# Optimization experiments

Hardware: AMD Instinct MI355X
Metric: run time of the kernel (lower is better)

## Reference

```python
import jax, jax.numpy as jnp
import numpy as np

R, S, RO, H, KD, VD = 14, 2, 7, 8, 32, 64  # resolution, stride, res_out, heads, key_dim, val_dim
EPS = 1e-5
SCALE = KD ** -0.5


def _bias_idxs():
    i = np.arange(R)
    kp = np.stack(np.meshgrid(i, i, indexing='ij')).reshape(2, -1)          # (2, 196)
    qi = np.arange(0, R, S)
    qp = np.stack(np.meshgrid(qi, qi, indexing='ij')).reshape(2, -1)        # (2, 49)
    rel = np.abs(qp[:, :, None] - kp[:, None, :])                           # (2, 49, 196)
    return jnp.asarray(rel[0] * R + rel[1], dtype=jnp.int32)                # (49, 196)

BIAS_IDXS = _bias_idxs()


def linear_norm(x, w, g, b, m, v):
    # Linear (no bias) followed by BatchNorm1d in eval mode (running stats)
    inv = g * jax.lax.rsqrt(v + EPS)
    return (x @ w.T) * inv + (b - m * inv)


def hardswish(x):
    return x * jnp.clip(x + 3.0, 0.0, 6.0) * (1.0 / 6.0)


def setup_inputs() -> dict:
    key = jax.random.key(0)
    ks = jax.random.split(key, 12)
    d = {
        'x': jax.random.normal(ks[0], (256, 196, 256), jnp.float32),
        'kv_w': jax.random.normal(ks[1], (768, 256), jnp.float32) * 0.02,
        'kv_g': jax.random.uniform(ks[2], (768,), jnp.float32, 0.5, 1.5),
        'kv_b': jax.random.normal(ks[3], (768,), jnp.float32) * 0.02,
        'kv_m': jax.random.normal(ks[4], (768,), jnp.float32) * 0.01,
        'kv_v': jax.random.uniform(ks[5], (768,), jnp.float32, 0.5, 1.5),
        'q_w': jax.random.normal(ks[6], (256, 256), jnp.float32) * 0.02,
        'q_g': jax.random.uniform(ks[7], (256,), jnp.float32, 0.5, 1.5),
        'q_b': jax.random.normal(ks[8], (256,), jnp.float32) * 0.02,
        'q_m': jax.random.normal(ks[9], (256,), jnp.float32) * 0.01,
        'q_v': jax.random.uniform(ks[10], (256,), jnp.float32, 0.5, 1.5),
        'proj_w': jax.random.normal(ks[11], (384, 512), jnp.float32) * 0.02,
        'proj_g': jnp.ones((384,), jnp.float32),
        'proj_b': jnp.zeros((384,), jnp.float32),
        'proj_m': jnp.zeros((384,), jnp.float32),
        'proj_v': jnp.ones((384,), jnp.float32),
        'attn_bias': jax.random.normal(jax.random.fold_in(key, 99), (H, R * R), jnp.float32) * 0.02,
    }
    return d


def reference(x, kv_w, kv_g, kv_b, kv_m, kv_v,
              q_w, q_g, q_b, q_m, q_v,
              proj_w, proj_g, proj_b, proj_m, proj_v, attn_bias):
    B, N, C = x.shape  # (B, 196, 256)
    kv = linear_norm(x, kv_w, kv_g, kv_b, kv_m, kv_v)          # (B, N, 768)
    kv = kv.reshape(B, N, H, KD + VD)                          # per-head split
    k = kv[..., :KD].transpose(0, 2, 3, 1)                     # (B, H, KD, N)
    v = kv[..., KD:].transpose(0, 2, 1, 3)                     # (B, H, N, VD)
    # Subsample queries on the 14x14 grid with stride 2 -> 49 tokens
    xq = x.reshape(B, R, R, C)[:, ::S, ::S].reshape(B, RO * RO, C)
    q = linear_norm(xq, q_w, q_g, q_b, q_m, q_v)               # (B, 49, 256)
    q = q.reshape(B, RO * RO, H, KD).transpose(0, 2, 1, 3)     # (B, H, 49, KD)
    bias = attn_bias[:, BIAS_IDXS]                             # (H, 49, 196)
    scores = jnp.einsum('bhqd,bhdn->bhqn', q, k) * SCALE + bias
    attn = jax.nn.softmax(scores, axis=-1)                     # (B, H, 49, 196)
    out = jnp.einsum('bhqn,bhnv->bhqv', attn, v)               # (B, H, 49, VD)
    out = out.transpose(0, 2, 1, 3).reshape(B, RO * RO, H * VD)  # (B, 49, 512)
    return linear_norm(hardswish(out), proj_w, proj_g, proj_b, proj_m, proj_v)  # (B, 49, 384)
```

## Files before the change

kernel.cpp:

```cpp
#include <hip/hip_runtime.h>

#define EPS 1e-5f
#define QK_SCALE 0.17677669529663687f

typedef __attribute__((ext_vector_type(8))) short bf16x8;
typedef __attribute__((ext_vector_type(4))) float f32x4;

__device__ inline unsigned short bf16_rne(float f) {
    unsigned int u = __float_as_uint(f);
    u = u + 0x7FFFu + ((u >> 16) & 1u);
    return (unsigned short)(u >> 16);
}
__device__ inline float bf16_f(unsigned short s) {
    return __uint_as_float(((unsigned int)s) << 16);
}
__device__ inline void split1(float v, unsigned short& hi, unsigned short& lo) {
    hi = bf16_rne(v); lo = bf16_rne(v - bf16_f(hi));
}

__device__ inline unsigned int cvtpk_bf16(float a, float b) {
    unsigned int r;
    asm("v_cvt_pk_bf16_f32 %0, %1, %2" : "=v"(r) : "v"(a), "v"(b));
    return r;
}
__device__ inline void split2pk(float a, float b, unsigned int& h, unsigned int& l) {
    h = cvtpk_bf16(a, b);
    float ra = a - __uint_as_float(h << 16);
    float rb = b - __uint_as_float(h & 0xFFFF0000u);
    l = cvtpk_bf16(ra, rb);
}
__device__ inline void split4pk(float4 v, uint2& h, uint2& l) {
    unsigned int h01, l01, h23, l23;
    split2pk(v.x, v.y, h01, l01);
    split2pk(v.z, v.w, h23, l23);
    h.x = h01; h.y = h23; l.x = l01; l.y = l23;
}

#define MFMA16(a, b, c) __builtin_amdgcn_mfma_f32_16x16x32_bf16((a), (b), (c), 0, 0, 0)

__global__ __launch_bounds__(256)
void prep_split(const float* __restrict__ kv_w, const float* __restrict__ q_w,
                const float* __restrict__ pw,
                unsigned short* __restrict__ wb_hi, unsigned short* __restrict__ wb_lo,
                unsigned short* __restrict__ pw_hi, unsigned short* __restrict__ pw_lo)
{
    int i = blockIdx.x * 256 + threadIdx.x;
    if (i < 262144) {
        int c = i & 255, j = (i >> 8) & 127, h = i >> 15;
        float v = (j < 96) ? kv_w[(h * 96 + j) * 256 + c]
                           : q_w[(h * 32 + (j - 96)) * 256 + c];
        unsigned short hi, lo; split1(v, hi, lo);
        wb_hi[i] = hi; wb_lo[i] = lo;
    } else {
        int p = i - 262144;
        if (p < 196608) {
            float v = pw[p];
            unsigned short hi, lo; split1(v, hi, lo);
            pw_hi[p] = hi; pw_lo[p] = lo;
        }
    }
}

__global__ __launch_bounds__(1024, 4)
void levit_fused_attn(const float* __restrict__ x,
                      const unsigned short* __restrict__ wb_hi,
                      const unsigned short* __restrict__ wb_lo,
                      const float* __restrict__ kv_g, const float* __restrict__ kv_b,
                      const float* __restrict__ kv_m, const float* __restrict__ kv_v,
                      const float* __restrict__ q_g, const float* __restrict__ q_b,
                      const float* __restrict__ q_m, const float* __restrict__ q_v,
                      const float* __restrict__ attn_bias,
                      unsigned short* __restrict__ ao_hi,
                      unsigned short* __restrict__ ao_lo)
{
    __shared__ __align__(16) unsigned short s_big[80192];
    __shared__ float bias_s[196];
    __shared__ float nrm_iv[128];
    __shared__ float nrm_be[128];

    unsigned short* s_phi = s_big;
    unsigned short* s_plo = s_big + 14848;
    unsigned short* s_khi = s_big + 29696;
    unsigned short* s_klo = s_big + 38016;
    unsigned short* s_qhi = s_big + 46336;
    unsigned short* s_qlo = s_big + 48416;
    unsigned short* s_vhi = s_big + 50496;
    unsigned short* s_vlo = s_big + 65344;
    unsigned short* st_xhi = s_big;
    unsigned short* st_xlo = s_big + 14976;
    unsigned short* st_whi = s_big + 29952;
    unsigned short* st_wlo = s_big + 39168;

    const int t = threadIdx.x;
    const int b = blockIdx.x;
    const int hh = blockIdx.y;

    const int l = t & 63;
    const int w = t >> 6;
    const int rg = w & 3;
    const int cg = w >> 2;
    const int lrow = l & 15;
    const int kg = (l >> 4) * 8;
    const int g4 = (l >> 4) * 4;

    const int x0row = t >> 3,  x0c8 = (t & 7) * 8;
    const int u1 = t + 1024;
    const int x1row = u1 >> 3, x1c8 = (u1 & 7) * 8;
    const bool xv1 = (t < 640);
    const int wj = t >> 3, wc8 = (t & 7) * 8;
    const unsigned short* wsrc_hi = wb_hi + (hh * 128 + wj) * 256 + wc8;
    const unsigned short* wsrc_lo = wb_lo + (hh * 128 + wj) * 256 + wc8;
    const float* xbase = x + b * 196 * 256;
    const float4 f4z = {0.f, 0.f, 0.f, 0.f};

    float4 x0a, x0b, x1a, x1b; bf16x8 wrh, wrl;

    x0a = (x0row < 196) ? *(const float4*)&xbase[x0row * 256 + x0c8]     : f4z;
    x0b = (x0row < 196) ? *(const float4*)&xbase[x0row * 256 + x0c8 + 4] : f4z;
    x1a = f4z; x1b = f4z;
    if (xv1 && x1row < 196) {
        x1a = *(const float4*)&xbase[x1row * 256 + x1c8];
        x1b = *(const float4*)&xbase[x1row * 256 + x1c8 + 4];
    }
    wrh = *(const bf16x8*)&wsrc_hi[0];
    wrl = *(const bf16x8*)&wsrc_lo[0];

    if (t < 196) bias_s[t] = attn_bias[hh * 196 + t];
    if (t >= 256 && t < 384) {
        int jj = t - 256;
        float gg, bb, mm, vv;
        if (jj < 96) { int col = hh * 96 + jj;        gg = kv_g[col]; bb = kv_b[col]; mm = kv_m[col]; vv = kv_v[col]; }
        else         { int col = hh * 32 + (jj - 96); gg = q_g[col];  bb = q_b[col];  mm = q_m[col];  vv = q_v[col]; }
        float iv = gg * rsqrtf(vv + EPS);
        nrm_iv[jj] = iv; nrm_be[jj] = bb - mm * iv;
    }
    for (int i = t; i < 64 * 36; i += 1024) {
        int r = i / 36, c = 196 + i % 36;
        s_vhi[r * 232 + c] = 0; s_vlo[r * 232 + c] = 0;
    }

    f32x4 acc[4][2];
    #pragma unroll
    for (int i = 0; i < 4; ++i) { acc[i][0] = (f32x4){0,0,0,0}; acc[i][1] = (f32x4){0,0,0,0}; }

    {
        uint2 ha, la, hb, lb;
        split4pk(x0a, ha, la); split4pk(x0b, hb, lb);
        *(uint4*)&st_xhi[x0row * 72 + x0c8] = (uint4){ha.x, ha.y, hb.x, hb.y};
        *(uint4*)&st_xlo[x0row * 72 + x0c8] = (uint4){la.x, la.y, lb.x, lb.y};
        if (xv1) {
            split4pk(x1a, ha, la); split4pk(x1b, hb, lb);
            *(uint4*)&st_xhi[x1row * 72 + x1c8] = (uint4){ha.x, ha.y, hb.x, hb.y};
            *(uint4*)&st_xlo[x1row * 72 + x1c8] = (uint4){la.x, la.y, lb.x, lb.y};
        }
    }
    *(bf16x8*)&st_whi[wj * 72 + wc8] = wrh;
    *(bf16x8*)&st_wlo[wj * 72 + wc8] = wrl;
    __syncthreads();

    for (int s = 0; s < 4; ++s) {
        if (s < 3) {
            const int kcn = 64 * (s + 1);
            x0a = (x0row < 196) ? *(const float4*)&xbase[x0row * 256 + kcn + x0c8]     : f4z;
            x0b = (x0row < 196) ? *(const float4*)&xbase[x0row * 256 + kcn + x0c8 + 4] : f4z;
            x1a = f4z; x1b = f4z;
            if (xv1 && x1row < 196) {
                x1a = *(const float4*)&xbase[x1row * 256 + kcn + x1c8];
                x1b = *(const float4*)&xbase[x1row * 256 + kcn + x1c8 + 4];
            }
            wrh = *(const bf16x8*)&wsrc_hi[kcn];
            wrl = *(const bf16x8*)&wsrc_lo[kcn];
        }

        #pragma unroll
        for (int sub = 0; sub < 2; ++sub) {
            const int ko = 32 * sub + kg;
            bf16x8 wfh[2], wfl[2];
            #pragma unroll
            for (int ctl = 0; ctl < 2; ++ctl) {
                const int jr = 16 * (2 * cg + ctl) + lrow;
                wfh[ctl] = *(const bf16x8*)&st_whi[jr * 72 + ko];
                wfl[ctl] = *(const bf16x8*)&st_wlo[jr * 72 + ko];
            }
            #pragma unroll
            for (int i = 0; i < 4; ++i) {
                const int rt = rg + 4 * i;
                if (rt < 13) {
                    const int arow = 16 * rt + lrow;
                    bf16x8 xh = *(const bf16x8*)&st_xhi[arow * 72 + ko];
                    bf16x8 xl = *(const bf16x8*)&st_xlo[arow * 72 + ko];
                    #pragma unroll
                    for (int ctl = 0; ctl < 2; ++ctl) {
                        acc[i][ctl] = MFMA16(wfh[ctl], xh, acc[i][ctl]);
                        acc[i][ctl] = MFMA16(wfh[ctl], xl, acc[i][ctl]);
                        acc[i][ctl] = MFMA16(wfl[ctl], xh, acc[i][ctl]);
                    }
                }
            }
        }

        if (s < 3) {
            uint4 h0, l0, h1, l1;
            {
                uint2 ha, la, hb, lb;
                split4pk(x0a, ha, la); split4pk(x0b, hb, lb);
                h0 = (uint4){ha.x, ha.y, hb.x, hb.y};
                l0 = (uint4){la.x, la.y, lb.x, lb.y};
                if (xv1) {
                    split4pk(x1a, ha, la); split4pk(x1b, hb, lb);
                    h1 = (uint4){ha.x, ha.y, hb.x, hb.y};
                    l1 = (uint4){la.x, la.y, lb.x, lb.y};
                }
            }
            __syncthreads();
            *(uint4*)&st_xhi[x0row * 72 + x0c8] = h0;
            *(uint4*)&st_xlo[x0row * 72 + x0c8] = l0;
            if (xv1) {
                *(uint4*)&st_xhi[x1row * 72 + x1c8] = h1;
                *(uint4*)&st_xlo[x1row * 72 + x1c8] = l1;
            }
            *(bf16x8*)&st_whi[wj * 72 + wc8] = wrh;
            *(bf16x8*)&st_wlo[wj * 72 + wc8] = wrl;
            __syncthreads();
        }
    }
    __syncthreads();

    #pragma unroll
    for (int ctl = 0; ctl < 2; ++ctl) {
        const int ct = 2 * cg + ctl;
        const int j0 = 16 * ct + g4;
        const float iv0 = nrm_iv[j0+0], be0 = nrm_be[j0+0];
        const float iv1 = nrm_iv[j0+1], be1 = nrm_be[j0+1];
        const float iv2 = nrm_iv[j0+2], be2 = nrm_be[j0+2];
        const float iv3 = nrm_iv[j0+3], be3 = nrm_be[j0+3];
        #pragma unroll
        for (int i = 0; i < 4; ++i) {
            const int rt = rg + 4 * i;
            if (rt < 13) {
                const int n = 16 * rt + lrow;
                if (n < 196) {
                    float v0 = acc[i][ctl][0] * iv0 + be0;
                    float v1 = acc[i][ctl][1] * iv1 + be1;
                    float v2 = acc[i][ctl][2] * iv2 + be2;
                    float v3 = acc[i][ctl][3] * iv3 + be3;
                    unsigned int h01, l01, h23, l23;
                    split2pk(v0, v1, h01, l01);
                    split2pk(v2, v3, h23, l23);
                    if (ct < 2) {
                        *(uint2*)&s_khi[n * 40 + j0] = (uint2){h01, h23};
                        *(uint2*)&s_klo[n * 40 + j0] = (uint2){l01, l23};
                    } else if (ct < 6) {
                        const int vd0 = j0 - 32;
                        s_vhi[(vd0+0) * 232 + n] = (unsigned short)h01;
                        s_vhi[(vd0+1) * 232 + n] = (unsigned short)(h01 >> 16);
                        s_vhi[(vd0+2) * 232 + n] = (unsigned short)h23;
                        s_vhi[(vd0+3) * 232 + n] = (unsigned short)(h23 >> 16);
                        s_vlo[(vd0+0) * 232 + n] = (unsigned short)l01;
                        s_vlo[(vd0+1) * 232 + n] = (unsigned short)(l01 >> 16);
                        s_vlo[(vd0+2) * 232 + n] = (unsigned short)l23;
                        s_vlo[(vd0+3) * 232 + n] = (unsigned short)(l23 >> 16);
                    } else {
                        const int a = n / 28, rem = n - 28 * a;
                        if (rem < 14 && !(rem & 1)) {
                            const int qi = a * 7 + (rem >> 1);
                            *(uint2*)&s_qhi[qi * 40 + (j0 - 96)] = (uint2){h01, h23};
                            *(uint2*)&s_qlo[qi * 40 + (j0 - 96)] = (uint2){l01, l23};
                        }
                    }
                }
            }
        }
    }
    __syncthreads();

    for (int i = t; i < 64 * 24; i += 1024) {
        int r = i / 24, c = 208 + i % 24;
        s_phi[r * 232 + c] = 0; s_plo[r * 232 + c] = 0;
    }

    if (w < 4) {
        const int mt = w;
        bf16x8 qh = *(const bf16x8*)&s_qhi[(16 * mt + lrow) * 40 + kg];
        bf16x8 ql = *(const bf16x8*)&s_qlo[(16 * mt + lrow) * 40 + kg];
        f32x4 sv[13];
        #pragma unroll
        for (int nt = 0; nt < 13; ++nt) {
            bf16x8 kh = *(const bf16x8*)&s_khi[(16 * nt + lrow) * 40 + kg];
            bf16x8 kl = *(const bf16x8*)&s_klo[(16 * nt + lrow) * 40 + kg];
            f32x4 a = {0.f, 0.f, 0.f, 0.f};
            a = MFMA16(kh, qh, a);
            a = MFMA16(kh, ql, a);
            a = MFMA16(kl, qh, a);
            sv[nt] = a;
        }
        const int m = 16 * mt + lrow;
        const int mq = m < 49 ? m : 48;
        const int yq = (mq / 7) * 2, xq2 = (mq % 7) * 2;

        float lmax = -3.0e38f;
        #pragma unroll
        for (int nt = 0; nt < 13; ++nt) {
            #pragma unroll
            for (int reg = 0; reg < 4; ++reg) {
                const int n = 16 * nt + g4 + reg;
                float sc;
                if (n < 196) {
                    const int yk = n / 14, xk = n - 14 * yk;
                    int d0 = yq - yk;  d0 = d0 < 0 ? -d0 : d0;
                    int d1 = xq2 - xk; d1 = d1 < 0 ? -d1 : d1;
                    sc = sv[nt][reg] * QK_SCALE + bias_s[d0 * 14 + d1];
                } else {
                    sc = -1.0e30f;
                }
                sv[nt][reg] = sc;
                lmax = fmaxf(lmax, sc);
            }
        }
        lmax = fmaxf(lmax, __shfl_xor(lmax, 16, 64));
        lmax = fmaxf(lmax, __shfl_xor(lmax, 32, 64));
        float rsum = 0.f;
        #pragma unroll
        for (int nt = 0; nt < 13; ++nt)
            #pragma unroll
            for (int reg = 0; reg < 4; ++reg) {
                float p = __expf(sv[nt][reg] - lmax);
                sv[nt][reg] = p;
                rsum += p;
            }
        rsum += __shfl_xor(rsum, 16, 64);
        rsum += __shfl_xor(rsum, 32, 64);
        const float rinv = 1.f / rsum;
        #pragma unroll
        for (int nt = 0; nt < 13; ++nt) {
            unsigned int h01, l01, h23, l23;
            split2pk(sv[nt][0] * rinv, sv[nt][1] * rinv, h01, l01);
            split2pk(sv[nt][2] * rinv, sv[nt][3] * rinv, h23, l23);
            const int o = m * 232 + 16 * nt + g4;
            *(uint2*)&s_phi[o] = (uint2){h01, h23};
            *(uint2*)&s_plo[o] = (uint2){l01, l23};
        }
    }
    __syncthreads();

    {
        const int mtv = w & 3;
        const int ntv = w >> 2;
        f32x4 pacc = {0.f, 0.f, 0.f, 0.f};
        #pragma unroll
        for (int s = 0; s < 7; ++s) {
            bf16x8 ph = *(const bf16x8*)&s_phi[(16 * mtv + lrow) * 232 + 32 * s + kg];
            bf16x8 pl = *(const bf16x8*)&s_plo[(16 * mtv + lrow) * 232 + 32 * s + kg];
            bf16x8 vh = *(const bf16x8*)&s_vhi[(16 * ntv + lrow) * 232 + 32 * s + kg];
            bf16x8 vl = *(const bf16x8*)&s_vlo[(16 * ntv + lrow) * 232 + 32 * s + kg];
            pacc = MFMA16(vh, ph, pacc);
            pacc = MFMA16(vh, pl, pacc);
            pacc = MFMA16(vl, ph, pacc);
        }
        const int m = 16 * mtv + lrow;
        if (m < 49) {
            const int vd0 = 16 * ntv + g4;
            float hs0, hs1, hs2, hs3;
            { float v = pacc[0]; hs0 = v * fminf(fmaxf(v + 3.f, 0.f), 6.f) * (1.f/6.f); }
            { float v = pacc[1]; hs1 = v * fminf(fmaxf(v + 3.f, 0.f), 6.f) * (1.f/6.f); }
            { float v = pacc[2]; hs2 = v * fminf(fmaxf(v + 3.f, 0.f), 6.f) * (1.f/6.f); }
            { float v = pacc[3]; hs3 = v * fminf(fmaxf(v + 3.f, 0.f), 6.f) * (1.f/6.f); }
            unsigned int h01, l01, h23, l23;
            split2pk(hs0, hs1, h01, l01);
            split2pk(hs2, hs3, h23, l23);
            const int idx = ((b * 49 + m) * 8 + hh) * 64 + vd0;
            *(uint2*)&ao_hi[idx] = (uint2){h01, h23};
            *(uint2*)&ao_lo[idx] = (uint2){l01, l23};
        }
    }
}

__global__ __launch_bounds__(512, 6)
void levit_proj(const unsigned short* __restrict__ ao_hi,
                const unsigned short* __restrict__ ao_lo,
                const unsigned short* __restrict__ pw_hi,
                const unsigned short* __restrict__ pw_lo,
                const float* __restrict__ pg, const float* __restrict__ pb,
                const float* __restrict__ pm, const float* __restrict__ pv,
                float* __restrict__ out)
{
    __shared__ __align__(16) unsigned short s_a[2 * 64 * 72];
    __shared__ __align__(16) unsigned short s_w[2 * 96 * 72];

    unsigned short* s_ahi = s_a;          unsigned short* s_alo = s_a + 64 * 72;
    unsigned short* s_whi = s_w;          unsigned short* s_wlo = s_w + 96 * 72;

    const int t = threadIdx.x;
    const int b = blockIdx.x;
    const int cg = blockIdx.y;
    const int l = t & 63;
    const int w = t >> 6;
    const int lrow = l & 15;
    const int kg = (l >> 4) * 8;
    const int g4 = (l >> 4) * 4;

    const int ar = t >> 3, ac8 = (t & 7) * 8;
    const bool aval = (ar < 49);
    const long aoff = (long)(b * 49 + ar) * 512 + ac8;
    int wpl_[3], wr_[3], wc_[3];
    #pragma unroll
    for (int it = 0; it < 3; ++it) {
        int f = t + 512 * it;
        int plane = (f >= 768), rem = plane ? f - 768 : f;
        wpl_[it] = plane; wr_[it] = rem >> 3; wc_[it] = (rem & 7) * 8;
    }

    bf16x8 pa_h = {}, pa_l = {}, pwr[3];

    if (aval) {
        pa_h = *(const bf16x8*)&ao_hi[aoff];
        pa_l = *(const bf16x8*)&ao_lo[aoff];
    }
    #pragma unroll
    for (int it = 0; it < 3; ++it) {
        const unsigned short* src = wpl_[it] ? pw_lo : pw_hi;
        pwr[it] = *(const bf16x8*)&src[(cg * 96 + wr_[it]) * 512 + wc_[it]];
    }
    *(bf16x8*)&s_ahi[ar * 72 + ac8] = pa_h;
    *(bf16x8*)&s_alo[ar * 72 + ac8] = pa_l;
    #pragma unroll
    for (int it = 0; it < 3; ++it) {
        unsigned short* dst = wpl_[it] ? s_wlo : s_whi;
        *(bf16x8*)&dst[wr_[it] * 72 + wc_[it]] = pwr[it];
    }
    __syncthreads();

    const int mt = w & 3;
    const int ntb = 3 * (w >> 2);

    f32x4 acc[3] = {{0.f,0.f,0.f,0.f},{0.f,0.f,0.f,0.f},{0.f,0.f,0.f,0.f}};

    for (int s = 0; s < 8; ++s) {
        if (s < 7) {
            const int kc = 64 * (s + 1);
            pa_h = (bf16x8){}; pa_l = (bf16x8){};
            if (aval) {
                pa_h = *(const bf16x8*)&ao_hi[aoff + kc];
                pa_l = *(const bf16x8*)&ao_lo[aoff + kc];
            }
            #pragma unroll
            for (int it = 0; it < 3; ++it) {
                const unsigned short* src = wpl_[it] ? pw_lo : pw_hi;
                pwr[it] = *(const bf16x8*)&src[(cg * 96 + wr_[it]) * 512 + kc + wc_[it]];
            }
        }

        #pragma unroll
        for (int sub = 0; sub < 2; ++sub) {
            const int ko = 32 * sub + kg;
            bf16x8 ah = *(const bf16x8*)&s_ahi[(16 * mt + lrow) * 72 + ko];
            bf16x8 al = *(const bf16x8*)&s_alo[(16 * mt + lrow) * 72 + ko];
            #pragma unroll
            for (int i = 0; i < 3; ++i) {
                const int nt = ntb + i;
                bf16x8 bh = *(const bf16x8*)&s_whi[(16 * nt + lrow) * 72 + ko];
                bf16x8 bl = *(const bf16x8*)&s_wlo[(16 * nt + lrow) * 72 + ko];
                acc[i] = MFMA16(bh, ah, acc[i]);
                acc[i] = MFMA16(bl, ah, acc[i]);
                acc[i] = MFMA16(bh, al, acc[i]);
            }
        }

        if (s < 7) {
            __syncthreads();
            *(bf16x8*)&s_ahi[ar * 72 + ac8] = pa_h;
            *(bf16x8*)&s_alo[ar * 72 + ac8] = pa_l;
            #pragma unroll
            for (int it = 0; it < 3; ++it) {
                unsigned short* dst = wpl_[it] ? s_wlo : s_whi;
                *(bf16x8*)&dst[wr_[it] * 72 + wc_[it]] = pwr[it];
            }
            __syncthreads();
        }
    }

    const int r = 16 * mt + lrow;
    if (r < 49) {
        #pragma unroll
        for (int i = 0; i < 3; ++i) {
            const int nt = ntb + i;
            const int o0 = cg * 96 + 16 * nt + g4;
            const float4 g4v = *(const float4*)&pg[o0];
            const float4 v4v = *(const float4*)&pv[o0];
            const float4 b4v = *(const float4*)&pb[o0];
            const float4 m4v = *(const float4*)&pm[o0];
            float iv0 = g4v.x * rsqrtf(v4v.x + EPS);
            float iv1 = g4v.y * rsqrtf(v4v.y + EPS);
            float iv2 = g4v.z * rsqrtf(v4v.z + EPS);
            float iv3 = g4v.w * rsqrtf(v4v.w + EPS);
            float4 ov;
            ov.x = acc[i][0] * iv0 + (b4v.x - m4v.x * iv0);
            ov.y = acc[i][1] * iv1 + (b4v.y - m4v.y * iv1);
            ov.z = acc[i][2] * iv2 + (b4v.z - m4v.z * iv2);
            ov.w = acc[i][3] * iv3 + (b4v.w - m4v.w * iv3);
            *(float4*)&out[(b * 49 + r) * 384 + o0] = ov;
        }
    }
}

extern "C" void kernel_launch(void* const* d_in, const int* in_sizes, int n_in,
                              void* d_out, int out_size, void* d_ws, size_t ws_size,
                              hipStream_t stream) {
    const float* x     = (const float*)d_in[0];
    const float* kv_w  = (const float*)d_in[1];
    const float* kv_g  = (const float*)d_in[2];
    const float* kv_b  = (const float*)d_in[3];
    const float* kv_m  = (const float*)d_in[4];
    const float* kv_v  = (const float*)d_in[5];
    const float* q_wp  = (const float*)d_in[6];
    const float* q_g   = (const float*)d_in[7];
    const float* q_b   = (const float*)d_in[8];
    const float* q_m   = (const float*)d_in[9];
    const float* q_v   = (const float*)d_in[10];
    const float* pw    = (const float*)d_in[11];
    const float* pg    = (const float*)d_in[12];
    const float* pb    = (const float*)d_in[13];
    const float* pm    = (const float*)d_in[14];
    const float* pv    = (const float*)d_in[15];
    const float* ab    = (const float*)d_in[16];

    unsigned short* ao_hi = (unsigned short*)d_ws;
    unsigned short* ao_lo = ao_hi + 12544 * 512;
    unsigned short* wb_hi = ao_lo + 12544 * 512;
    unsigned short* wb_lo = wb_hi + 262144;
    unsigned short* pw_hi = wb_lo + 262144;
    unsigned short* pw_lo = pw_hi + 196608;

    prep_split<<<1792, 256, 0, stream>>>(kv_w, q_wp, pw, wb_hi, wb_lo, pw_hi, pw_lo);

    dim3 g1(256, 8);
    levit_fused_attn<<<g1, 1024, 0, stream>>>(x, wb_hi, wb_lo,
                                              kv_g, kv_b, kv_m, kv_v,
                                              q_g, q_b, q_m, q_v, ab, ao_hi, ao_lo);
    levit_proj<<<dim3(256, 4), 512, 0, stream>>>(ao_hi, ao_lo, pw_hi, pw_lo,
                                                 pg, pb, pm, pv, (float*)d_out);
}
```

Measured before the change: 281.9 us.

## Process two heads per block to reuse staged x tiles across heads

Each attention block now computes the KV/Q projection for two heads, staging 256 weight rows per K-step instead of 128, and the grid is halved along the head axis. This halves how often each fp32 x tile is read from global memory and split into bf16 hi/lo. The attention and PV stages then run the two heads one after another inside the block. Norm parameters are now read from global memory in the epilogue instead of being precomputed in shared memory. In exchange, the block keeps twice as many accumulators live, which raises register pressure, and the grid has fewer blocks.

```diff
diff --git a/kernel.cpp b/kernel.cpp
--- a/kernel.cpp
+++ b/kernel.cpp
@@ -74,9 +74,7 @@
                       unsigned short* __restrict__ ao_lo)
 {
     __shared__ __align__(16) unsigned short s_big[80192];
-    __shared__ float bias_s[196];
-    __shared__ float nrm_iv[128];
-    __shared__ float nrm_be[128];
+    __shared__ float bias_s[392];
 
     unsigned short* s_phi = s_big;
     unsigned short* s_plo = s_big + 14848;
@@ -89,11 +87,11 @@
     unsigned short* st_xhi = s_big;
     unsigned short* st_xlo = s_big + 14976;
     unsigned short* st_whi = s_big + 29952;
-    unsigned short* st_wlo = s_big + 39168;
+    unsigned short* st_wlo = s_big + 48384;
 
     const int t = threadIdx.x;
     const int b = blockIdx.x;
-    const int hh = blockIdx.y;
+    const int hp = blockIdx.y;
 
     const int l = t & 63;
     const int w = t >> 6;
@@ -107,13 +105,14 @@
     const int u1 = t + 1024;
     const int x1row = u1 >> 3, x1c8 = (u1 & 7) * 8;
     const bool xv1 = (t < 640);
-    const int wj = t >> 3, wc8 = (t & 7) * 8;
-    const unsigned short* wsrc_hi = wb_hi + (hh * 128 + wj) * 256 + wc8;
-    const unsigned short* wsrc_lo = wb_lo + (hh * 128 + wj) * 256 + wc8;
+    const int wj0 = t >> 3, wc8 = (t & 7) * 8;
+    const unsigned short* wsrc_hi = wb_hi + (hp * 256 + wj0) * 256 + wc8;
+    const unsigned short* wsrc_lo = wb_lo + (hp * 256 + wj0) * 256 + wc8;
     const float* xbase = x + b * 196 * 256;
     const float4 f4z = {0.f, 0.f, 0.f, 0.f};
 
-    float4 x0a, x0b, x1a, x1b; bf16x8 wrh, wrl;
+    float4 x0a, x0b, x1a, x1b;
+    bf16x8 wrh0, wrl0, wrh1, wrl1;
 
     x0a = (x0row < 196) ? *(const float4*)&xbase[x0row * 256 + x0c8]     : f4z;
     x0b = (x0row < 196) ? *(const float4*)&xbase[x0row * 256 + x0c8 + 4] : f4z;
@@ -122,26 +121,21 @@
         x1a = *(const float4*)&xbase[x1row * 256 + x1c8];
         x1b = *(const float4*)&xbase[x1row * 256 + x1c8 + 4];
     }
-    wrh = *(const bf16x8*)&wsrc_hi[0];
-    wrl = *(const bf16x8*)&wsrc_lo[0];
-
-    if (t < 196) bias_s[t] = attn_bias[hh * 196 + t];
-    if (t >= 256 && t < 384) {
-        int jj = t - 256;
-        float gg, bb, mm, vv;
-        if (jj < 96) { int col = hh * 96 + jj;        gg = kv_g[col]; bb = kv_b[col]; mm = kv_m[col]; vv = kv_v[col]; }
-        else         { int col = hh * 32 + (jj - 96); gg = q_g[col];  bb = q_b[col];  mm = q_m[col];  vv = q_v[col]; }
-        float iv = gg * rsqrtf(vv + EPS);
-        nrm_iv[jj] = iv; nrm_be[jj] = bb - mm * iv;
-    }
-    for (int i = t; i < 64 * 36; i += 1024) {
-        int r = i / 36, c = 196 + i % 36;
-        s_vhi[r * 232 + c] = 0; s_vlo[r * 232 + c] = 0;
-    }
-
-    f32x4 acc[4][2];
+    wrh0 = *(const bf16x8*)&wsrc_hi[0];
+    wrl0 = *(const bf16x8*)&wsrc_lo[0];
+    wrh1 = *(const bf16x8*)&wsrc_hi[128 * 256];
+    wrl1 = *(const bf16x8*)&wsrc_lo[128 * 256];
+
+    if (t < 392) {
+        int h2 = (t >= 196), idx = t - 196 * h2;
+        bias_s[t] = attn_bias[(2 * hp + h2) * 196 + idx];
+    }
+
+    f32x4 acc[4][4];
     #pragma unroll
-    for (int i = 0; i < 4; ++i) { acc[i][0] = (f32x4){0,0,0,0}; acc[i][1] = (f32x4){0,0,0,0}; }
+    for (int i = 0; i < 4; ++i)
+        #pragma unroll
+        for (int k = 0; k < 4; ++k) acc[i][k] = (f32x4){0,0,0,0};
 
     {
         uint2 ha, la, hb, lb;
@@ -154,8 +148,10 @@
             *(uint4*)&st_xlo[x1row * 72 + x1c8] = (uint4){la.x, la.y, lb.x, lb.y};
         }
     }
-    *(bf16x8*)&st_whi[wj * 72 + wc8] = wrh;
-    *(bf16x8*)&st_wlo[wj * 72 + wc8] = wrl;
+    *(bf16x8*)&st_whi[wj0 * 72 + wc8] = wrh0;
+    *(bf16x8*)&st_wlo[wj0 * 72 + wc8] = wrl0;
+    *(bf16x8*)&st_whi[(wj0 + 128) * 72 + wc8] = wrh1;
+    *(bf16x8*)&st_wlo[(wj0 + 128) * 72 + wc8] = wrl1;
     __syncthreads();
 
     for (int s = 0; s < 4; ++s) {
@@ -168,20 +164,25 @@
                 x1a = *(const float4*)&xbase[x1row * 256 + kcn + x1c8];
                 x1b = *(const float4*)&xbase[x1row * 256 + kcn + x1c8 + 4];
             }
-            wrh = *(const bf16x8*)&wsrc_hi[kcn];
-            wrl = *(const bf16x8*)&wsrc_lo[kcn];
+            wrh0 = *(const bf16x8*)&wsrc_hi[kcn];
+            wrl0 = *(const bf16x8*)&wsrc_lo[kcn];
+            wrh1 = *(const bf16x8*)&wsrc_hi[128 * 256 + kcn];
+            wrl1 = *(const bf16x8*)&wsrc_lo[128 * 256 + kcn];
         }
 
         #pragma unroll
         for (int sub = 0; sub < 2; ++sub) {
             const int ko = 32 * sub + kg;
-            bf16x8 wfh[2], wfl[2];
-            #pragma unroll
-            for (int ctl = 0; ctl < 2; ++ctl) {
-                const int jr = 16 * (2 * cg + ctl) + lrow;
-                wfh[ctl] = *(const bf16x8*)&st_whi[jr * 72 + ko];
-                wfl[ctl] = *(const bf16x8*)&st_wlo[jr * 72 + ko];
-            }
+            bf16x8 wfh[4], wfl[4];
+            #pragma unroll
+            for (int h2 = 0; h2 < 2; ++h2)
+                #pragma unroll
+                for (int ctl = 0; ctl < 2; ++ctl) {
+                    const int k = 2 * h2 + ctl;
+                    const int jr = h2 * 128 + 16 * (2 * cg + ctl) + lrow;
+                    wfh[k] = *(const bf16x8*)&st_whi[jr * 72 + ko];
+                    wfl[k] = *(const bf16x8*)&st_wlo[jr * 72 + ko];
+                }
             #pragma unroll
             for (int i = 0; i < 4; ++i) {
                 const int rt = rg + 4 * i;
@@ -190,10 +191,10 @@
                     bf16x8 xh = *(const bf16x8*)&st_xhi[arow * 72 + ko];
                     bf16x8 xl = *(const bf16x8*)&st_xlo[arow * 72 + ko];
                     #pragma unroll
-                    for (int ctl = 0; ctl < 2; ++ctl) {
-                        acc[i][ctl] = MFMA16(wfh[ctl], xh, acc[i][ctl]);
-                        acc[i][ctl] = MFMA16(wfh[ctl], xl, acc[i][ctl]);
-                        acc[i][ctl] = MFMA16(wfl[ctl], xh, acc[i][ctl]);
+                    for (int k = 0; k < 4; ++k) {
+                        acc[i][k] = MFMA16(wfh[k], xh, acc[i][k]);
+                        acc[i][k] = MFMA16(wfh[k], xl, acc[i][k]);
+                        acc[i][k] = MFMA16(wfl[k], xh, acc[i][k]);
                     }
                 }
             }
@@ -219,159 +220,185 @@
                 *(uint4*)&st_xhi[x1row * 72 + x1c8] = h1;
                 *(uint4*)&st_xlo[x1row * 72 + x1c8] = l1;
             }
-            *(bf16x8*)&st_whi[wj * 72 + wc8] = wrh;
-            *(bf16x8*)&st_wlo[wj * 72 + wc8] = wrl;
+            *(bf16x8*)&st_whi[wj0 * 72 + wc8] = wrh0;
+            *(bf16x8*)&st_wlo[wj0 * 72 + wc8] = wrl0;
+            *(bf16x8*)&st_whi[(wj0 + 128) * 72 + wc8] = wrh1;
+            *(bf16x8*)&st_wlo[(wj0 + 128) * 72 + wc8] = wrl1;
             __syncthreads();
         }
     }
     __syncthreads();
 
     #pragma unroll
-    for (int ctl = 0; ctl < 2; ++ctl) {
-        const int ct = 2 * cg + ctl;
-        const int j0 = 16 * ct + g4;
-        const float iv0 = nrm_iv[j0+0], be0 = nrm_be[j0+0];
-        const float iv1 = nrm_iv[j0+1], be1 = nrm_be[j0+1];
-        const float iv2 = nrm_iv[j0+2], be2 = nrm_be[j0+2];
-        const float iv3 = nrm_iv[j0+3], be3 = nrm_be[j0+3];
+    for (int h = 0; h < 2; ++h) {
+        const int head = 2 * hp + h;
+
         #pragma unroll
-        for (int i = 0; i < 4; ++i) {
-            const int rt = rg + 4 * i;
-            if (rt < 13) {
-                const int n = 16 * rt + lrow;
-                if (n < 196) {
-                    float v0 = acc[i][ctl][0] * iv0 + be0;
-                    float v1 = acc[i][ctl][1] * iv1 + be1;
-                    float v2 = acc[i][ctl][2] * iv2 + be2;
-                    float v3 = acc[i][ctl][3] * iv3 + be3;
-                    unsigned int h01, l01, h23, l23;
-                    split2pk(v0, v1, h01, l01);
-                    split2pk(v2, v3, h23, l23);
-                    if (ct < 2) {
-                        *(uint2*)&s_khi[n * 40 + j0] = (uint2){h01, h23};
-                        *(uint2*)&s_klo[n * 40 + j0] = (uint2){l01, l23};
-                    } else if (ct < 6) {
-                        const int vd0 = j0 - 32;
-                        s_vhi[(vd0+0) * 232 + n] = (unsigned short)h01;
-                        s_vhi[(vd0+1) * 232 + n] = (unsigned short)(h01 >> 16);
-                        s_vhi[(vd0+2) * 232 + n] = (unsigned short)h23;
-                        s_vhi[(vd0+3) * 232 + n] = (unsigned short)(h23 >> 16);
-                        s_vlo[(vd0+0) * 232 + n] = (unsigned short)l01;
-                        s_vlo[(vd0+1) * 232 + n] = (unsigned short)(l01 >> 16);
-                        s_vlo[(vd0+2) * 232 + n] = (unsigned short)l23;
-                        s_vlo[(vd0+3) * 232 + n] = (unsigned short)(l23 >> 16);
-                    } else {
-                        const int a = n / 28, rem = n - 28 * a;
-                        if (rem < 14 && !(rem & 1)) {
-                            const int qi = a * 7 + (rem >> 1);
-                            *(uint2*)&s_qhi[qi * 40 + (j0 - 96)] = (uint2){h01, h23};
-                            *(uint2*)&s_qlo[qi * 40 + (j0 - 96)] = (uint2){l01, l23};
+        for (int ctl = 0; ctl < 2; ++ctl) {
+            const int ct = 2 * cg + ctl;
+            const int k = 2 * h + ctl;
+            const int j0 = 16 * ct + g4;
+            float4 gv, bv, mv, vv;
+            if (ct < 6) {
+                const int col = head * 96 + j0;
+                gv = *(const float4*)&kv_g[col]; bv = *(const float4*)&kv_b[col];
+                mv = *(const float4*)&kv_m[col]; vv = *(const float4*)&kv_v[col];
+            } else {
+                const int col = head * 32 + (j0 - 96);
+                gv = *(const float4*)&q_g[col]; bv = *(const float4*)&q_b[col];
+                mv = *(const float4*)&q_m[col]; vv = *(const float4*)&q_v[col];
+            }
+            const float iv0 = gv.x * rsqrtf(vv.x + EPS), be0 = bv.x - mv.x * iv0;
+            const float iv1 = gv.y * rsqrtf(vv.y + EPS), be1 = bv.y - mv.y * iv1;
+            const float iv2 = gv.z * rsqrtf(vv.z + EPS), be2 = bv.z - mv.z * iv2;
+            const float iv3 = gv.w * rsqrtf(vv.w + EPS), be3 = bv.w - mv.w * iv3;
+            #pragma unroll
+            for (int i = 0; i < 4; ++i) {
+                const int rt = rg + 4 * i;
+                if (rt < 13) {
+                    const int n = 16 * rt + lrow;
+                    if (n < 196) {
+                        float v0 = acc[i][k][0] * iv0 + be0;
+                        float v1 = acc[i][k][1] * iv1 + be1;
+                        float v2 = acc[i][k][2] * iv2 + be2;
+                        float v3 = acc[i][k][3] * iv3 + be3;
+                        unsigned int h01, l01, h23, l23;
+                        split2pk(v0, v1, h01, l01);
+                        split2pk(v2, v3, h23, l23);
+                        if (ct < 2) {
+                            *(uint2*)&s_khi[n * 40 + j0] = (uint2){h01, h23};
+                            *(uint2*)&s_klo[n * 40 + j0] = (uint2){l01, l23};
+                        } else if (ct < 6) {
+                            const int vd0 = j0 - 32;
+                            s_vhi[(vd0+0) * 232 + n] = (unsigned short)h01;
+                            s_vhi[(vd0+1) * 232 + n] = (unsigned short)(h01 >> 16);
+                            s_vhi[(vd0+2) * 232 + n] = (unsigned short)h23;
+                            s_vhi[(vd0+3) * 232 + n] = (unsigned short)(h23 >> 16);
+                            s_vlo[(vd0+0) * 232 + n] = (unsigned short)l01;
+                            s_vlo[(vd0+1) * 232 + n] = (unsigned short)(l01 >> 16);
+                            s_vlo[(vd0+2) * 232 + n] = (unsigned short)l23;
+                            s_vlo[(vd0+3) * 232 + n] = (unsigned short)(l23 >> 16);
+                        } else {
+                            const int a = n / 28, rem = n - 28 * a;
+                            if (rem < 14 && !(rem & 1)) {
+                                const int qi = a * 7 + (rem >> 1);
+                                *(uint2*)&s_qhi[qi * 40 + (j0 - 96)] = (uint2){h01, h23};
+                                *(uint2*)&s_qlo[qi * 40 + (j0 - 96)] = (uint2){l01, l23};
+                            }
                         }
                     }
                 }
             }
         }
-    }
-    __syncthreads();
-
-    for (int i = t; i < 64 * 24; i += 1024) {
-        int r = i / 24, c = 208 + i % 24;
-        s_phi[r * 232 + c] = 0; s_plo[r * 232 + c] = 0;
-    }
-
-    if (w < 4) {
-        const int mt = w;
-        bf16x8 qh = *(const bf16x8*)&s_qhi[(16 * mt + lrow) * 40 + kg];
-        bf16x8 ql = *(const bf16x8*)&s_qlo[(16 * mt + lrow) * 40 + kg];
-        f32x4 sv[13];
-        #pragma unroll
-        for (int nt = 0; nt < 13; ++nt) {
-            bf16x8 kh = *(const bf16x8*)&s_khi[(16 * nt + lrow) * 40 + kg];
-            bf16x8 kl = *(const bf16x8*)&s_klo[(16 * nt + lrow) * 40 + kg];
-            f32x4 a = {0.f, 0.f, 0.f, 0.f};
-            a = MFMA16(kh, qh, a);
-            a = MFMA16(kh, ql, a);
-            a = MFMA16(kl, qh, a);
-            sv[nt] = a;
-        }
-        const int m = 16 * mt + lrow;
-        const int mq = m < 49 ? m : 48;
-        const int yq = (mq / 7) * 2, xq2 = (mq % 7) * 2;
-
-        float lmax = -3.0e38f;
-        #pragma unroll
-        for (int nt = 0; nt < 13; ++nt) {
-            #pragma unroll
-            for (int reg = 0; reg < 4; ++reg) {
-                const int n = 16 * nt + g4 + reg;
-                float sc;
-                if (n < 196) {
-                    const int yk = n / 14, xk = n - 14 * yk;
-                    int d0 = yq - yk;  d0 = d0 < 0 ? -d0 : d0;
-                    int d1 = xq2 - xk; d1 = d1 < 0 ? -d1 : d1;
-                    sc = sv[nt][reg] * QK_SCALE + bias_s[d0 * 14 + d1];
-                } else {
-                    sc = -1.0e30f;
+        if (h == 0) {
+            for (int i = t; i < 64 * 36; i += 1024) {
+                int r = i / 36, c = 196 + i % 36;
+                s_vhi[r * 232 + c] = 0; s_vlo[r * 232 + c] = 0;
+            }
+        }
+        __syncthreads();
+
+        if (w < 4) {
+            const int mt = w;
+            bf16x8 qh = *(const bf16x8*)&s_qhi[(16 * mt + lrow) * 40 + kg];
+            bf16x8 ql = *(const bf16x8*)&s_qlo[(16 * mt + lrow) * 40 + kg];
+            f32x4 sv[13];
+            #pragma unroll
+            for (int nt = 0; nt < 13; ++nt) {
+                bf16x8 kh = *(const bf16x8*)&s_khi[(16 * nt + lrow) * 40 + kg];
+                bf16x8 kl = *(const bf16x8*)&s_klo[(16 * nt + lrow) * 40 + kg];
+                f32x4 a = {0.f, 0.f, 0.f, 0.f};
+                a = MFMA16(kh, qh, a);
+                a = MFMA16(kh, ql, a);
+                a = MFMA16(kl, qh, a);
+                sv[nt] = a;
+            }
+            const int m = 16 * mt + lrow;
+            const int mq = m < 49 ? m : 48;
+            const int yq = (mq / 7) * 2, xq2 = (mq % 7) * 2;
+            const float* bias_h = bias_s + h * 196;
+
+            float lmax = -3.0e38f;
+            #pragma unroll
+            for (int nt = 0; nt < 13; ++nt) {
+                #pragma unroll
+                for (int reg = 0; reg < 4; ++reg) {
+                    const int n = 16 * nt + g4 + reg;
+                    float sc;
+                    if (n < 196) {
+                        const int yk = n / 14, xk = n - 14 * yk;
+                        int d0 = yq - yk;  d0 = d0 < 0 ? -d0 : d0;
+                        int d1 = xq2 - xk; d1 = d1 < 0 ? -d1 : d1;
+                        sc = sv[nt][reg] * QK_SCALE + bias_h[d0 * 14 + d1];
+                    } else {
+                        sc = -1.0e30f;
+                    }
+                    sv[nt][reg] = sc;
+                    lmax = fmaxf(lmax, sc);
                 }
-                sv[nt][reg] = sc;
-                lmax = fmaxf(lmax, sc);
-            }
-        }
-        lmax = fmaxf(lmax, __shfl_xor(lmax, 16, 64));
-        lmax = fmaxf(lmax, __shfl_xor(lmax, 32, 64));
-        float rsum = 0.f;
-        #pragma unroll
-        for (int nt = 0; nt < 13; ++nt)
-            #pragma unroll
-            for (int reg = 0; reg < 4; ++reg) {
-                float p = __expf(sv[nt][reg] - lmax);
-                sv[nt][reg] = p;
-                rsum += p;
-            }
-        rsum += __shfl_xor(rsum, 16, 64);
-        rsum += __shfl_xor(rsum, 32, 64);
-        const float rinv = 1.f / rsum;
-        #pragma unroll
-        for (int nt = 0; nt < 13; ++nt) {
-            unsigned int h01, l01, h23, l23;
-            split2pk(sv[nt][0] * rinv, sv[nt][1] * rinv, h01, l01);
-            split2pk(sv[nt][2] * rinv, sv[nt][3] * rinv, h23, l23);
-            const int o = m * 232 + 16 * nt + g4;
-            *(uint2*)&s_phi[o] = (uint2){h01, h23};
-            *(uint2*)&s_plo[o] = (uint2){l01, l23};
-        }
-    }
-    __syncthreads();
-
-    {
-        const int mtv = w & 3;
-        const int ntv = w >> 2;
-        f32x4 pacc = {0.f, 0.f, 0.f, 0.f};
-        #pragma unroll
-        for (int s = 0; s < 7; ++s) {
-            bf16x8 ph = *(const bf16x8*)&s_phi[(16 * mtv + lrow) * 232 + 32 * s + kg];
-            bf16x8 pl = *(const bf16x8*)&s_plo[(16 * mtv + lrow) * 232 + 32 * s + kg];
-            bf16x8 vh = *(const bf16x8*)&s_vhi[(16 * ntv + lrow) * 232 + 32 * s + kg];
-            bf16x8 vl = *(const bf16x8*)&s_vlo[(16 * ntv + lrow) * 232 + 32 * s + kg];
-            pacc = MFMA16(vh, ph, pacc);
-            pacc = MFMA16(vh, pl, pacc);
-            pacc = MFMA16(vl, ph, pacc);
-        }
-        const int m = 16 * mtv + lrow;
-        if (m < 49) {
-            const int vd0 = 16 * ntv + g4;
-            float hs0, hs1, hs2, hs3;
-            { float v = pacc[0]; hs0 = v * fminf(fmaxf(v + 3.f, 0.f), 6.f) * (1.f/6.f); }
-            { float v = pacc[1]; hs1 = v * fminf(fmaxf(v + 3.f, 0.f), 6.f) * (1.f/6.f); }
-            { float v = pacc[2]; hs2 = v * fminf(fmaxf(v + 3.f, 0.f), 6.f) * (1.f/6.f); }
-            { float v = pacc[3]; hs3 = v * fminf(fmaxf(v + 3.f, 0.f), 6.f) * (1.f/6.f); }
-            unsigned int h01, l01, h23, l23;
-            split2pk(hs0, hs1, h01, l01);
-            split2pk(hs2, hs3, h23, l23);
-            const int idx = ((b * 49 + m) * 8 + hh) * 64 + vd0;
-            *(uint2*)&ao_hi[idx] = (uint2){h01, h23};
-            *(uint2*)&ao_lo[idx] = (uint2){l01, l23};
-        }
+            }
+            lmax = fmaxf(lmax, __shfl_xor(lmax, 16, 64));
+            lmax = fmaxf(lmax, __shfl_xor(lmax, 32, 64));
+            float rsum = 0.f;
+            #pragma unroll
+            for (int nt = 0; nt < 13; ++nt)
+                #pragma unroll
+                for (int reg = 0; reg < 4; ++reg) {
+                    float p = __expf(sv[nt][reg] - lmax);
+                    sv[nt][reg] = p;
+                    rsum += p;
+                }
+            rsum += __shfl_xor(rsum, 16, 64);
+            rsum += __shfl_xor(rsum, 32, 64);
+            const float rinv = 1.f / rsum;
+            #pragma unroll
+            for (int nt = 0; nt < 13; ++nt) {
+                unsigned int h01, l01, h23, l23;
+                split2pk(sv[nt][0] * rinv, sv[nt][1] * rinv, h01, l01);
+                split2pk(sv[nt][2] * rinv, sv[nt][3] * rinv, h23, l23);
+                const int o = m * 232 + 16 * nt + g4;
+                *(uint2*)&s_phi[o] = (uint2){h01, h23};
+                *(uint2*)&s_plo[o] = (uint2){l01, l23};
+            }
+        } else if (h == 0) {
+            for (int i = t - 256; i < 64 * 24; i += 768) {
+                int r = i / 24, c = 208 + i % 24;
+                s_phi[r * 232 + c] = 0; s_plo[r * 232 + c] = 0;
+            }
+        }
+        __syncthreads();
+
+        {
+            const int mtv = w & 3;
+            const int ntv = w >> 2;
+            f32x4 pacc = {0.f, 0.f, 0.f, 0.f};
+            #pragma unroll
+            for (int s = 0; s < 7; ++s) {
+                bf16x8 ph = *(const bf16x8*)&s_phi[(16 * mtv + lrow) * 232 + 32 * s + kg];
+                bf16x8 pl = *(const bf16x8*)&s_plo[(16 * mtv + lrow) * 232 + 32 * s + kg];
+                bf16x8 vh = *(const bf16x8*)&s_vhi[(16 * ntv + lrow) * 232 + 32 * s + kg];
+                bf16x8 vl = *(const bf16x8*)&s_vlo[(16 * ntv + lrow) * 232 + 32 * s + kg];
+                pacc = MFMA16(vh, ph, pacc);
+                pacc = MFMA16(vh, pl, pacc);
+                pacc = MFMA16(vl, ph, pacc);
+            }
+            const int m = 16 * mtv + lrow;
+            if (m < 49) {
+                const int vd0 = 16 * ntv + g4;
+                float hs0, hs1, hs2, hs3;
+                { float v = pacc[0]; hs0 = v * fminf(fmaxf(v + 3.f, 0.f), 6.f) * (1.f/6.f); }
+                { float v = pacc[1]; hs1 = v * fminf(fmaxf(v + 3.f, 0.f), 6.f) * (1.f/6.f); }
+                { float v = pacc[2]; hs2 = v * fminf(fmaxf(v + 3.f, 0.f), 6.f) * (1.f/6.f); }
+                { float v = pacc[3]; hs3 = v * fminf(fmaxf(v + 3.f, 0.f), 6.f) * (1.f/6.f); }
+                unsigned int h01, l01, h23, l23;
+                split2pk(hs0, hs1, h01, l01);
+                split2pk(hs2, hs3, h23, l23);
+                const int idx = ((b * 49 + m) * 8 + head) * 64 + vd0;
+                *(uint2*)&ao_hi[idx] = (uint2){h01, h23};
+                *(uint2*)&ao_lo[idx] = (uint2){l01, l23};
+            }
+        }
+        if (h == 0) __syncthreads();
     }
 }
 
@@ -533,7 +560,7 @@
 
     prep_split<<<1792, 256, 0, stream>>>(kv_w, q_wp, pw, wb_hi, wb_lo, pw_hi, pw_lo);
 
-    dim3 g1(256, 8);
+    dim3 g1(256, 4);
     levit_fused_attn<<<g1, 1024, 0, stream>>>(x, wb_hi, wb_lo,
                                               kv_g, kv_b, kv_m, kv_v,
                                               q_g, q_b, q_m, q_v, ab, ao_hi, ao_lo);
```

New measurement: 500.5 us. 77.5% more time.
